# Performance work log

Hardware: AMD Instinct MI355X
Metric: run time of the kernel (lower is better)

## Reference

```python
import jax, jax.numpy as jnp
import numpy as np

D_MODEL, D_LOW, NUM_BINS = 512, 64, 39
DIST_MIN, DIST_MAX = 2.0, 22.0
BIN_WIDTH = (DIST_MAX - DIST_MIN) / (NUM_BINS - 1)
LN_EPS = 1e-5


def setup_inputs() -> dict:
    key = jax.random.key(0)
    ks = jax.random.split(key, 10)
    B, N = 2, 768
    h_res = jax.random.normal(ks[0], (B, N, D_MODEL), dtype=jnp.float32)
    # scale coords so pairwise distances span the [2, 22] bin range
    x_true = jax.random.normal(ks[1], (B, N, 3), dtype=jnp.float32) * 5.0
    token_pad_mask = jnp.ones((B, N), dtype=jnp.float32)
    s = 1.0 / np.sqrt(D_MODEL)
    return {
        "h_res": h_res,
        "x_true": x_true,
        "token_pad_mask": token_pad_mask,
        "ln_w": jnp.ones((D_MODEL,), jnp.float32),
        "ln_b": jnp.zeros((D_MODEL,), jnp.float32),
        "wu_w": jax.random.normal(ks[2], (D_LOW, D_MODEL), jnp.float32) * s,
        "wu_b": jnp.zeros((D_LOW,), jnp.float32),
        "wv_w": jax.random.normal(ks[3], (D_LOW, D_MODEL), jnp.float32) * s,
        "wv_b": jnp.zeros((D_LOW,), jnp.float32),
        "wb_w": jax.random.normal(ks[4], (NUM_BINS, D_LOW), jnp.float32) * (1.0 / np.sqrt(D_LOW)),
        "wb_b": jnp.zeros((NUM_BINS,), jnp.float32),
    }


def _layernorm(x, w, b):
    mu = jnp.mean(x, axis=-1, keepdims=True)
    var = jnp.mean(jnp.square(x - mu), axis=-1, keepdims=True)
    return (x - mu) * jax.lax.rsqrt(var + LN_EPS) * w + b


def reference(h_res, x_true, token_pad_mask, ln_w, ln_b, wu_w, wu_b, wv_w, wv_b, wb_w, wb_b):
    B, N, _ = h_res.shape
    # pairwise distances -> target bins (trunc-to-int then clamp, as torch .long())
    diff = x_true[:, :, None, :] - x_true[:, None, :, :]          # [B,N,N,3]
    d_true = jnp.sqrt(jnp.sum(diff * diff, axis=-1))               # [B,N,N]
    target = jnp.clip(((d_true - DIST_MIN) / BIN_WIDTH).astype(jnp.int32), 0, NUM_BINS - 1)

    h = _layernorm(h_res, ln_w, ln_b)
    U = h @ wu_w.T + wu_b                                          # [B,N,d_low]
    V = h @ wv_w.T + wv_b                                          # [B,N,d_low]
    # logits[b,i,j,k] = sum_c U[b,i,c] V[b,j,c] Wb[k,c] + bb[k]
    logits = jnp.einsum("bic,bjc,kc->bijk", U, V, wb_w) + wb_b     # [B,N,N,K]
    logp = jax.nn.log_softmax(logits, axis=-1)
    ce = -jnp.take_along_axis(logp, target[..., None], axis=-1)[..., 0]  # [B,N,N]

    mask = (token_pad_mask[:, :, None] * token_pad_mask[:, None, :]) > 0  # [B,N,N] bool
    counts = jnp.sum(mask, axis=(1, 2))                            # [B]
    per_sample = jnp.sum(jnp.where(mask, ce, 0.0), axis=(1, 2)) / jnp.maximum(counts, 1)
    valid = counts > 0
    total_count = jnp.sum(valid)
    loss = jnp.sum(jnp.where(valid, per_sample, 0.0)) / jnp.maximum(total_count, 1)
    return loss
```

## Files before the change

kernel.cpp:

```cpp
#include <hip/hip_runtime.h>
#include <hip/hip_bf16.h>
#include <math.h>

#define D_MODEL 512
#define D_LOW   64
#define NBINS   39
#define LOG2E   1.4426950408889634f
#define LN2     0.6931471805599453f

typedef __attribute__((ext_vector_type(8))) short short8;
typedef __attribute__((ext_vector_type(4))) float floatx4;

__global__ __launch_bounds__(256) void lnproj_tbin_kernel(
    const float* __restrict__ h_res,
    const float* __restrict__ ln_w, const float* __restrict__ ln_b,
    const float* __restrict__ wu_w, const float* __restrict__ wu_b,
    const float* __restrict__ wv_w, const float* __restrict__ wv_b,
    const float* __restrict__ x_true, const float* __restrict__ pmask,
    float* __restrict__ U, __hip_bfloat16* __restrict__ Vbf,
    signed char* __restrict__ tbg, int N, int B, int nLN, int TB) {
  const int tid = threadIdx.x;

  if ((int)blockIdx.x >= nLN) {
    const int idx   = blockIdx.x - nLN;
    const int NN    = N * N;
    const int total = B * NN;
    const float BW  = (22.0f - 2.0f) / 38.0f;
    for (int p = idx * 256 + tid; p < total; p += TB * 256) {
      const int b = p / NN;
      const int r = p - b * NN;
      const int i = r / N;
      const int j = r - i * N;
      const int rowi = b * N + i, rowj = b * N + j;
      const float dx = x_true[rowi * 3 + 0] - x_true[rowj * 3 + 0];
      const float dy = x_true[rowi * 3 + 1] - x_true[rowj * 3 + 1];
      const float dz = x_true[rowi * 3 + 2] - x_true[rowj * 3 + 2];
      const float d  = sqrtf(dx * dx + dy * dy + dz * dz);
      int tb = (int)((d - 2.0f) / BW);
      tb = tb < 0 ? 0 : (tb > NBINS - 1 ? NBINS - 1 : tb);
      const bool ok = (pmask[rowi] * pmask[rowj]) > 0.f;
      tbg[p] = ok ? (signed char)tb : (signed char)-1;
    }
    return;
  }

  const int wave = tid >> 6, lane = tid & 63;
  const int q = lane >> 4, ln16 = lane & 15;
  const int row0 = blockIdx.x * 16;
  const float* hp = h_res + (size_t)(row0 + ln16) * D_MODEL + q * 8;

  short8 abf[16];
  float sum = 0.f, ssq = 0.f;
  #pragma unroll
  for (int kc = 0; kc < 16; ++kc) {
    const floatx4 x0 = *reinterpret_cast<const floatx4*>(hp + kc * 32);
    const floatx4 x1 = *reinterpret_cast<const floatx4*>(hp + kc * 32 + 4);
    short8 a;
    #pragma unroll
    for (int e = 0; e < 4; ++e) {
      sum += x0[e]; ssq += x0[e] * x0[e];
      const __hip_bfloat16 hb = __float2bfloat16(x0[e]);
      a[e] = *reinterpret_cast<const short*>(&hb);
    }
    #pragma unroll
    for (int e = 0; e < 4; ++e) {
      sum += x1[e]; ssq += x1[e] * x1[e];
      const __hip_bfloat16 hb = __float2bfloat16(x1[e]);
      a[4 + e] = *reinterpret_cast<const short*>(&hb);
    }
    abf[kc] = a;
  }
  sum += __shfl_xor(sum, 16); sum += __shfl_xor(sum, 32);
  ssq += __shfl_xor(ssq, 16); ssq += __shfl_xor(ssq, 32);
  const float mu  = sum * (1.0f / (float)D_MODEL);
  const float var = ssq * (1.0f / (float)D_MODEL) - mu * mu;
  const float rs  = rsqrtf(var + 1e-5f);
  float mu_r[4], rs_r[4];
  #pragma unroll
  for (int r = 0; r < 4; ++r) {
    mu_r[r] = __shfl(mu, q * 4 + r);
    rs_r[r] = __shfl(rs, q * 4 + r);
  }

  const int obase = wave * 32;
  const int out0 = obase + ln16;
  const int out1 = obase + 16 + ln16;
  const float* wr0 = (out0 < 64) ? (wu_w + out0 * D_MODEL) : (wv_w + (out0 - 64) * D_MODEL);
  const float* wr1 = (out1 < 64) ? (wu_w + out1 * D_MODEL) : (wv_w + (out1 - 64) * D_MODEL);
  const float sc0 = (out0 < 64) ? LOG2E : 1.0f;
  const float sc1 = (out1 < 64) ? LOG2E : 1.0f;

  floatx4 acc0 = (floatx4){0.f, 0.f, 0.f, 0.f};
  floatx4 acc1 = (floatx4){0.f, 0.f, 0.f, 0.f};
  float s1a = 0.f, s1b = 0.f;
  float s2a = 0.f, s2b = 0.f;
  #pragma unroll
  for (int kc = 0; kc < 16; ++kc) {
    const int c0 = kc * 32 + q * 8;
    const floatx4 lw0 = *reinterpret_cast<const floatx4*>(ln_w + c0);
    const floatx4 lw1 = *reinterpret_cast<const floatx4*>(ln_w + c0 + 4);
    const floatx4 lb0 = *reinterpret_cast<const floatx4*>(ln_b + c0);
    const floatx4 lb1 = *reinterpret_cast<const floatx4*>(ln_b + c0 + 4);
    const floatx4 wa0 = *reinterpret_cast<const floatx4*>(wr0 + c0);
    const floatx4 wa1 = *reinterpret_cast<const floatx4*>(wr0 + c0 + 4);
    const floatx4 wb0 = *reinterpret_cast<const floatx4*>(wr1 + c0);
    const floatx4 wb1 = *reinterpret_cast<const floatx4*>(wr1 + c0 + 4);
    short8 b0, b1;
    #pragma unroll
    for (int e = 0; e < 4; ++e) {
      const float v0 = wa0[e] * lw0[e] * sc0;
      const float v1 = wa1[e] * lw1[e] * sc0;
      const __hip_bfloat16 h0 = __float2bfloat16(v0);
      const __hip_bfloat16 h1 = __float2bfloat16(v1);
      b0[e]     = *reinterpret_cast<const short*>(&h0);
      b0[4 + e] = *reinterpret_cast<const short*>(&h1);
      s1a += __bfloat162float(h0) + __bfloat162float(h1);
      s2a += wa0[e] * lb0[e] + wa1[e] * lb1[e];
      const float u0 = wb0[e] * lw0[e] * sc1;
      const float u1 = wb1[e] * lw1[e] * sc1;
      const __hip_bfloat16 g0 = __float2bfloat16(u0);
      const __hip_bfloat16 g1 = __float2bfloat16(u1);
      b1[e]     = *reinterpret_cast<const short*>(&g0);
      b1[4 + e] = *reinterpret_cast<const short*>(&g1);
      s1b += __bfloat162float(g0) + __bfloat162float(g1);
      s2b += wb0[e] * lb0[e] + wb1[e] * lb1[e];
    }
    acc0 = __builtin_amdgcn_mfma_f32_16x16x32_bf16(abf[kc], b0, acc0, 0, 0, 0);
    acc1 = __builtin_amdgcn_mfma_f32_16x16x32_bf16(abf[kc], b1, acc1, 0, 0, 0);
  }
  s1a += __shfl_xor(s1a, 16); s1a += __shfl_xor(s1a, 32);
  s1b += __shfl_xor(s1b, 16); s1b += __shfl_xor(s1b, 32);
  s2a += __shfl_xor(s2a, 16); s2a += __shfl_xor(s2a, 32);
  s2b += __shfl_xor(s2b, 16); s2b += __shfl_xor(s2b, 32);
  const float bias0 = sc0 * (((out0 < 64) ? wu_b[out0] : wv_b[out0 - 64]) + s2a);
  const float bias1 = sc1 * (((out1 < 64) ? wu_b[out1] : wv_b[out1 - 64]) + s2b);

  #pragma unroll
  for (int nt = 0; nt < 2; ++nt) {
    const int out  = nt ? out1 : out0;
    const floatx4 a = nt ? acc1 : acc0;
    const float ws = nt ? s1b : s1a;
    const float bb = nt ? bias1 : bias0;
    #pragma unroll
    for (int r = 0; r < 4; ++r) {
      const int rowg = row0 + q * 4 + r;
      const float val = rs_r[r] * a[r] - mu_r[r] * rs_r[r] * ws + bb;
      if (out < 64) {
        U[(size_t)rowg * D_LOW + out] = val;
      } else {
        Vbf[(size_t)rowg * D_LOW + (out - 64)] = __float2bfloat16(val);
      }
    }
  }
}

__global__ __launch_bounds__(256) void pair_mfma_kernel(
    const float* __restrict__ U,
    const __hip_bfloat16* __restrict__ Vbf,
    const float* __restrict__ wb_w, const float* __restrict__ wb_b,
    const signed char* __restrict__ tbg,
    float* __restrict__ part, int N) {
  __shared__ float rbuf[8];
  const int i = blockIdx.x, b = blockIdx.y;
  const int tid  = threadIdx.x;
  const int wave = tid >> 6, lane = tid & 63;
  const int q = lane >> 4, ln16 = lane & 15;
  const int rowi = b * N + i;

  short8 wfrag[3][2];
  {
    const float* Up = U + (size_t)rowi * D_LOW;
    #pragma unroll
    for (int t = 0; t < 3; ++t) {
      const int n = t * 16 + ln16;
      #pragma unroll
      for (int s = 0; s < 2; ++s) {
        const int c0 = s * 32 + q * 8;
        short8 f;
        #pragma unroll
        for (int e = 0; e < 8; ++e) {
          const float w = (n < NBINS) ? wb_w[n * D_LOW + c0 + e] : 0.f;
          const float v = Up[c0 + e] * w;
          const __hip_bfloat16 hb = __float2bfloat16(v);
          f[e] = *reinterpret_cast<const short*>(&hb);
        }
        wfrag[t][s] = f;
      }
    }
  }

  float bias2[3][4];
  #pragma unroll
  for (int t = 0; t < 3; ++t)
    #pragma unroll
    for (int r = 0; r < 4; ++r) {
      const int bin = t * 16 + q * 4 + r;
      bias2[t][r] = (bin < NBINS) ? LOG2E * wb_b[bin] : -INFINITY;
    }

  const short* Vp = reinterpret_cast<const short*>(Vbf) + (size_t)b * N * D_LOW;
  const signed char* tbp = tbg + (size_t)b * N * N + (size_t)i * N;
  float ce_sum = 0.f, cnt_sum = 0.f;

  for (int g = 0; g < 6; ++g) {
    const int jb = wave * 192 + g * 32;

    short8 v[2][2];
    int tbv[2];
    #pragma unroll
    for (int tt = 0; tt < 2; ++tt) {
      const size_t jr = jb + tt * 16 + ln16;
      v[tt][0] = *reinterpret_cast<const short8*>(Vp + jr * D_LOW + q * 8);
      v[tt][1] = *reinterpret_cast<const short8*>(Vp + jr * D_LOW + 32 + q * 8);
      tbv[tt]  = (int)tbp[jr];
    }

    floatx4 f[2][3];
    #pragma unroll
    for (int tt = 0; tt < 2; ++tt)
      #pragma unroll
      for (int t = 0; t < 3; ++t) {
        floatx4 a = (floatx4){0.f, 0.f, 0.f, 0.f};
        a = __builtin_amdgcn_mfma_f32_16x16x32_bf16(wfrag[t][0], v[tt][0], a, 0, 0, 0);
        a = __builtin_amdgcn_mfma_f32_16x16x32_bf16(wfrag[t][1], v[tt][1], a, 0, 0, 0);
        f[tt][t] = a;
      }

    #pragma unroll
    for (int tt = 0; tt < 2; ++tt) {
      const int tb = tbv[tt];
      float ssum = 0.f, lt = 0.f;
      #pragma unroll
      for (int t = 0; t < 3; ++t)
        #pragma unroll
        for (int r = 0; r < 4; ++r) {
          const float l2 = f[tt][t][r] + bias2[t][r];
          ssum += __builtin_amdgcn_exp2f(l2);
          lt += (t * 16 + q * 4 + r == tb) ? l2 : 0.f;
        }
      ssum += __shfl_xor(ssum, 16); ssum += __shfl_xor(ssum, 32);
      const float ok = (tb >= 0) ? 1.f : 0.f;
      ce_sum  += ok * LN2 * (__builtin_amdgcn_logf(ssum) - 4.0f * lt);
      cnt_sum += ok;
    }
  }

  #pragma unroll
  for (int off = 32; off; off >>= 1) {
    ce_sum  += __shfl_xor(ce_sum, off);
    cnt_sum += __shfl_xor(cnt_sum, off);
  }
  if (lane == 0) { rbuf[wave] = ce_sum; rbuf[4 + wave] = cnt_sum; }
  __syncthreads();
  if (tid == 0) {
    part[rowi * 2 + 0] = rbuf[0] + rbuf[1] + rbuf[2] + rbuf[3];
    part[rowi * 2 + 1] = rbuf[4] + rbuf[5] + rbuf[6] + rbuf[7];
  }
}

__global__ __launch_bounds__(256) void finalize_kernel(
    const float* __restrict__ part, float* __restrict__ out, int N, int B) {
  __shared__ float red[8];
  const int tid = threadIdx.x, wave = tid >> 6, lane = tid & 63;
  float loss = 0.f, vcount = 0.f;
  for (int b = 0; b < B; ++b) {
    float ce = 0.f, cnt = 0.f;
    for (int i = tid; i < N; i += 256) {
      ce  += part[(b * N + i) * 2 + 0];
      cnt += part[(b * N + i) * 2 + 1];
    }
    #pragma unroll
    for (int off = 32; off; off >>= 1) {
      ce  += __shfl_xor(ce, off);
      cnt += __shfl_xor(cnt, off);
    }
    if (lane == 0) { red[wave] = ce; red[4 + wave] = cnt; }
    __syncthreads();
    if (tid == 0) {
      const float s = red[0] + red[1] + red[2] + red[3];
      const float c = red[4] + red[5] + red[6] + red[7];
      if (c > 0.f) { loss += s / fmaxf(c, 1.f); vcount += 1.f; }
    }
    __syncthreads();
  }
  if (tid == 0) out[0] = (vcount > 0.f) ? loss / vcount : 0.f;
}

extern "C" void kernel_launch(void* const* d_in, const int* in_sizes, int n_in,
                              void* d_out, int out_size, void* d_ws, size_t ws_size,
                              hipStream_t stream) {
  const float* h_res  = (const float*)d_in[0];
  const float* x_true = (const float*)d_in[1];
  const float* pmask  = (const float*)d_in[2];
  const float* ln_w   = (const float*)d_in[3];
  const float* ln_b   = (const float*)d_in[4];
  const float* wu_w   = (const float*)d_in[5];
  const float* wu_b   = (const float*)d_in[6];
  const float* wv_w   = (const float*)d_in[7];
  const float* wv_b   = (const float*)d_in[8];
  const float* wb_w   = (const float*)d_in[9];
  const float* wb_b   = (const float*)d_in[10];

  const int B  = 2;
  const int N  = in_sizes[2] / B;
  const int BN = B * N;
  const int nLN = BN / 16;
  const int TB  = 160;

  float* U = (float*)d_ws;
  __hip_bfloat16* Vbf = (__hip_bfloat16*)(U + (size_t)BN * D_LOW);
  float* part = (float*)(Vbf + (size_t)BN * D_LOW);
  signed char* tbg = (signed char*)(part + 2 * (size_t)BN);

  lnproj_tbin_kernel<<<nLN + TB, 256, 0, stream>>>(
      h_res, ln_w, ln_b, wu_w, wu_b, wv_w, wv_b, x_true, pmask,
      U, Vbf, tbg, N, B, nLN, TB);
  pair_mfma_kernel<<<dim3(N, B), 256, 0, stream>>>(U, Vbf, wb_w, wb_b, tbg,
                                                   part, N);
  finalize_kernel<<<1, 256, 0, stream>>>(part, (float*)d_out, N, B);
}
```

Baseline: 124.4 us.

## Split pair kernel j-range across two blocks, prefetch V, fold bias into MFMA

Doubles the pair-kernel grid so each block covers half the j range, with each wave now doing 3 groups instead of 6. Next-group V fragments and target bins are loaded one iteration ahead so the loads overlap the MFMA and exp work. The bias is used as the MFMA accumulator's starting value, and the softmax sum is split across four accumulators. The cost is that every block redoes the per-row wfrag setup, and the partial buffer and finalize loop double in size.

```diff
diff --git a/kernel.cpp b/kernel.cpp
--- a/kernel.cpp
+++ b/kernel.cpp
@@ -161,7 +161,9 @@
     const signed char* __restrict__ tbg,
     float* __restrict__ part, int N) {
   __shared__ float rbuf[8];
-  const int i = blockIdx.x, b = blockIdx.y;
+  const int i    = blockIdx.x;
+  const int b    = blockIdx.y >> 1;
+  const int half = blockIdx.y & 1;
   const int tid  = threadIdx.x;
   const int wave = tid >> 6, lane = tid & 63;
   const int q = lane >> 4, ln16 = lane & 15;
@@ -189,38 +191,54 @@
     }
   }
 
-  float bias2[3][4];
+  floatx4 bias_init[3];
   #pragma unroll
   for (int t = 0; t < 3; ++t)
     #pragma unroll
     for (int r = 0; r < 4; ++r) {
       const int bin = t * 16 + q * 4 + r;
-      bias2[t][r] = (bin < NBINS) ? LOG2E * wb_b[bin] : -INFINITY;
+      bias_init[t][r] = (bin < NBINS) ? LOG2E * wb_b[bin] : -INFINITY;
     }
 
   const short* Vp = reinterpret_cast<const short*>(Vbf) + (size_t)b * N * D_LOW;
   const signed char* tbp = tbg + (size_t)b * N * N + (size_t)i * N;
+  const int jbase = half * 384 + wave * 96;
+  const int q4 = q * 4;
+
   float ce_sum = 0.f, cnt_sum = 0.f;
 
-  for (int g = 0; g < 6; ++g) {
-    const int jb = wave * 192 + g * 32;
-
-    short8 v[2][2];
-    int tbv[2];
+  short8 v[2][2];
+  int tbv[2];
+  {
     #pragma unroll
     for (int tt = 0; tt < 2; ++tt) {
-      const size_t jr = jb + tt * 16 + ln16;
+      const size_t jr = jbase + tt * 16 + ln16;
       v[tt][0] = *reinterpret_cast<const short8*>(Vp + jr * D_LOW + q * 8);
       v[tt][1] = *reinterpret_cast<const short8*>(Vp + jr * D_LOW + 32 + q * 8);
       tbv[tt]  = (int)tbp[jr];
     }
+  }
+
+  for (int g = 0; g < 3; ++g) {
+    short8 vn[2][2];
+    int tbn[2];
+    if (g < 2) {
+      const int jb = jbase + (g + 1) * 32;
+      #pragma unroll
+      for (int tt = 0; tt < 2; ++tt) {
+        const size_t jr = jb + tt * 16 + ln16;
+        vn[tt][0] = *reinterpret_cast<const short8*>(Vp + jr * D_LOW + q * 8);
+        vn[tt][1] = *reinterpret_cast<const short8*>(Vp + jr * D_LOW + 32 + q * 8);
+        tbn[tt]   = (int)tbp[jr];
+      }
+    }
 
     floatx4 f[2][3];
     #pragma unroll
     for (int tt = 0; tt < 2; ++tt)
       #pragma unroll
       for (int t = 0; t < 3; ++t) {
-        floatx4 a = (floatx4){0.f, 0.f, 0.f, 0.f};
+        floatx4 a = bias_init[t];
         a = __builtin_amdgcn_mfma_f32_16x16x32_bf16(wfrag[t][0], v[tt][0], a, 0, 0, 0);
         a = __builtin_amdgcn_mfma_f32_16x16x32_bf16(wfrag[t][1], v[tt][1], a, 0, 0, 0);
         f[tt][t] = a;
@@ -228,21 +246,34 @@
 
     #pragma unroll
     for (int tt = 0; tt < 2; ++tt) {
-      const int tb = tbv[tt];
-      float ssum = 0.f, lt = 0.f;
-      #pragma unroll
-      for (int t = 0; t < 3; ++t)
-        #pragma unroll
-        for (int r = 0; r < 4; ++r) {
-          const float l2 = f[tt][t][r] + bias2[t][r];
-          ssum += __builtin_amdgcn_exp2f(l2);
-          lt += (t * 16 + q * 4 + r == tb) ? l2 : 0.f;
-        }
+      const int tb  = tbv[tt];
+      const int tbq = tb - q4;
+      float s0 = 0.f, s1 = 0.f, s2 = 0.f, s3 = 0.f, lt = 0.f;
+      #pragma unroll
+      for (int t = 0; t < 3; ++t) {
+        const floatx4 fv = f[tt][t];
+        s0 += __builtin_amdgcn_exp2f(fv[0]);
+        s1 += __builtin_amdgcn_exp2f(fv[1]);
+        s2 += __builtin_amdgcn_exp2f(fv[2]);
+        s3 += __builtin_amdgcn_exp2f(fv[3]);
+        lt += (tbq == t * 16 + 0) ? fv[0] : 0.f;
+        lt += (tbq == t * 16 + 1) ? fv[1] : 0.f;
+        lt += (tbq == t * 16 + 2) ? fv[2] : 0.f;
+        lt += (tbq == t * 16 + 3) ? fv[3] : 0.f;
+      }
+      float ssum = (s0 + s1) + (s2 + s3);
       ssum += __shfl_xor(ssum, 16); ssum += __shfl_xor(ssum, 32);
       const float ok = (tb >= 0) ? 1.f : 0.f;
       ce_sum  += ok * LN2 * (__builtin_amdgcn_logf(ssum) - 4.0f * lt);
       cnt_sum += ok;
     }
+
+    if (g < 2) {
+      #pragma unroll
+      for (int tt = 0; tt < 2; ++tt) {
+        v[tt][0] = vn[tt][0]; v[tt][1] = vn[tt][1]; tbv[tt] = tbn[tt];
+      }
+    }
   }
 
   #pragma unroll
@@ -253,8 +284,9 @@
   if (lane == 0) { rbuf[wave] = ce_sum; rbuf[4 + wave] = cnt_sum; }
   __syncthreads();
   if (tid == 0) {
-    part[rowi * 2 + 0] = rbuf[0] + rbuf[1] + rbuf[2] + rbuf[3];
-    part[rowi * 2 + 1] = rbuf[4] + rbuf[5] + rbuf[6] + rbuf[7];
+    const size_t slot = ((size_t)(b * 2 + half) * N + i) * 2;
+    part[slot + 0] = rbuf[0] + rbuf[1] + rbuf[2] + rbuf[3];
+    part[slot + 1] = rbuf[4] + rbuf[5] + rbuf[6] + rbuf[7];
   }
 }
 
@@ -265,9 +297,10 @@
   float loss = 0.f, vcount = 0.f;
   for (int b = 0; b < B; ++b) {
     float ce = 0.f, cnt = 0.f;
-    for (int i = tid; i < N; i += 256) {
-      ce  += part[(b * N + i) * 2 + 0];
-      cnt += part[(b * N + i) * 2 + 1];
+    for (int e = tid; e < 2 * N; e += 256) {
+      const size_t base = ((size_t)b * 2 * N + e) * 2;
+      ce  += part[base + 0];
+      cnt += part[base + 1];
     }
     #pragma unroll
     for (int off = 32; off; off >>= 1) {
@@ -310,12 +343,12 @@
   float* U = (float*)d_ws;
   __hip_bfloat16* Vbf = (__hip_bfloat16*)(U + (size_t)BN * D_LOW);
   float* part = (float*)(Vbf + (size_t)BN * D_LOW);
-  signed char* tbg = (signed char*)(part + 2 * (size_t)BN);
+  signed char* tbg = (signed char*)(part + 4 * (size_t)BN);
 
   lnproj_tbin_kernel<<<nLN + TB, 256, 0, stream>>>(
       h_res, ln_w, ln_b, wu_w, wu_b, wv_w, wv_b, x_true, pmask,
       U, Vbf, tbg, N, B, nLN, TB);
-  pair_mfma_kernel<<<dim3(N, B), 256, 0, stream>>>(U, Vbf, wb_w, wb_b, tbg,
-                                                   part, N);
+  pair_mfma_kernel<<<dim3(N, 2 * B), 256, 0, stream>>>(U, Vbf, wb_w, wb_b,
+                                                       tbg, part, N);
   finalize_kernel<<<1, 256, 0, stream>>>(part, (float*)d_out, N, B);
 }
```

After: 134.8 us. +8.4%, slower.
